# Kernel tuning notes

Measured on AMD Instinct MI355X. Metric: run time of the kernel, lower is better.

Reference implementation:

```python
import jax, jax.numpy as jnp
import numpy as np


def _ln(x, g, b, eps=1e-5):
    m = x.mean(-1, keepdims=True)
    v = x.var(-1, keepdims=True)
    return (x - m) / jnp.sqrt(v + eps) * g + b


def setup_inputs() -> dict:
    key = jax.random.key(0)
    ks = iter(jax.random.split(key, 48))
    B, N, H, Ld, L, FF = 2048, 10, 256, 8, 4, 1024
    def w(shape, s=0.02):
        return jax.random.normal(next(ks), shape, jnp.float32) * s
    return dict(
        latent_code=jax.random.normal(next(ks), (B, Ld), jnp.float32),
        target_node_types=jax.random.randint(next(ks), (B, N), 0, 5),
        ce_w1=w((Ld, H)), ce_b1=jnp.zeros(H), ce_g1=jnp.ones(H), ce_be1=jnp.zeros(H),
        ce_w2=w((H, H)), ce_b2=jnp.zeros(H), ce_g2=jnp.ones(H), ce_be2=jnp.zeros(H),
        nc_w1=w((2, H // 4)), nc_b1=jnp.zeros(H // 4), nc_w2=w((H // 4, 3)), nc_b2=jnp.zeros(3),
        type_emb=w((5, H), 1.0), pos_emb=w((N, H), 0.02),
        qkvo_w=w((L, 4, H, H)), qkvo_b=jnp.zeros((L, 4, H)),
        ln_g=jnp.ones((L, 2, H)), ln_b=jnp.zeros((L, 2, H)),
        ffn_w1=w((L, H, FF)), ffn_b1=jnp.zeros((L, FF)),
        ffn_w2=w((L, FF, H)), ffn_b2=jnp.zeros((L, H)),
        out_w=w((H, 5)), out_b=jnp.zeros(5),
        edge_w1=w((2 * H + Ld, H)), edge_b1=jnp.zeros(H),
        edge_w2=w((H, 8)), edge_b2=jnp.zeros(8),
    )


def reference(latent_code, target_node_types,
              ce_w1, ce_b1, ce_g1, ce_be1, ce_w2, ce_b2, ce_g2, ce_be2,
              nc_w1, nc_b1, nc_w2, nc_b2,
              type_emb, pos_emb, qkvo_w, qkvo_b, ln_g, ln_b,
              ffn_w1, ffn_b1, ffn_w2, ffn_b2, out_w, out_b,
              edge_w1, edge_b1, edge_w2, edge_b2):
    B, Ld = latent_code.shape
    N = target_node_types.shape[1]
    H = ce_w1.shape[1]
    L = qkvo_w.shape[0]
    nh = 8
    hd = H // nh

    # context encoder: Linear -> LN -> ReLU -> Linear -> LN
    h0 = jax.nn.relu(_ln(latent_code @ ce_w1 + ce_b1, ce_g1, ce_be1))
    context = _ln(h0 @ ce_w2 + ce_b2, ce_g2, ce_be2)  # [B,H]

    # node count head on latent_code[:, :2]
    node_count_logits = jax.nn.relu(latent_code[:, :2] @ nc_w1 + nc_b1) @ nc_w2 + nc_b2  # [B,3]

    # teacher-forced node embeddings (independent of predictions -> vectorizable)
    ne = type_emb[target_node_types] + pos_emb[:N]          # [B,N,H]
    h = context[:, None, :] + pos_emb[:N]                   # queries [B,N,H]
    mem = jnp.concatenate([context[:, None, :], ne], axis=1)  # keys [B,N+1,H]
    # position i attends to context (k=0) and nodes j<i (k=j+1), i.e. k <= i
    kmask = (jnp.arange(N + 1)[None, :] <= jnp.arange(N)[:, None])  # [N,N+1]
    scale = 1.0 / np.sqrt(hd).astype(np.float32)

    for l in range(L):
        Q = (h @ qkvo_w[l, 0] + qkvo_b[l, 0]).reshape(B, N, nh, hd)
        K = (mem @ qkvo_w[l, 1] + qkvo_b[l, 1]).reshape(B, N + 1, nh, hd)
        V = (mem @ qkvo_w[l, 2] + qkvo_b[l, 2]).reshape(B, N + 1, nh, hd)
        s = jnp.einsum('bnhd,bmhd->bhnm', Q, K) * scale
        s = jnp.where(kmask[None, None], s, jnp.float32(-1e9))
        a = jax.nn.softmax(s, axis=-1)
        o = jnp.einsum('bhnm,bmhd->bnhd', a, V).reshape(B, N, H)
        h = _ln(h + o @ qkvo_w[l, 3] + qkvo_b[l, 3], ln_g[l, 0], ln_b[l, 0])
        f = jax.nn.relu(h @ ffn_w1[l] + ffn_b1[l]) @ ffn_w2[l] + ffn_b2[l]
        h = _ln(h + f, ln_g[l, 1], ln_b[l, 1])

    node_logits = h @ out_w + out_b  # [B,N,5]

    # pairwise edge decoder on (emb_i, emb_j, latent) for i>j, symmetrized
    ei = jnp.broadcast_to(ne[:, :, None, :], (B, N, N, H))
    ej = jnp.broadcast_to(ne[:, None, :, :], (B, N, N, H))
    lat = jnp.broadcast_to(latent_code[:, None, None, :], (B, N, N, Ld))
    feat = jnp.concatenate([ei, ej, lat], axis=-1)  # [B,N,N,2H+Ld]
    elog = jax.nn.relu(feat @ edge_w1 + edge_b1) @ edge_w2 + edge_b2  # [B,N,N,8]
    tril = (jnp.arange(N)[:, None] > jnp.arange(N)[None, :])[None, :, :, None]
    lower = jnp.where(tril, elog, jnp.float32(0.0))
    edge_component_logits = lower + jnp.swapaxes(lower, 1, 2)  # diag stays zero

    return node_logits, node_count_logits, edge_component_logits
```

## Files before the change

kernel.cpp:

```cpp
#include <hip/hip_runtime.h>
#include <hip/hip_bf16.h>

#define BATCH 2048
#define NNODE 10
#define NLAYER 4
#define ROWS_H (BATCH*NNODE)
#define ROWS_M (BATCH*(NNODE+1))
#define KVSTR 2048

typedef __hip_bfloat16 bf16;
typedef unsigned short u16;
typedef unsigned int u32;
typedef __attribute__((ext_vector_type(8))) short bf16x8;
typedef __attribute__((ext_vector_type(4))) float f32x4;

__device__ __forceinline__ float bfb(u16 u) {
    union { u32 i; float f; } c; c.i = (u32)u << 16; return c.f;
}
__device__ __forceinline__ float bf2f(bf16 x) { return __bfloat162float(x); }
__device__ __forceinline__ bf16 f2bf(float x) { return __float2bfloat16(x); }
__device__ __forceinline__ u16 f2u(float v) {
    bf16 t = f2bf(v); u16 u; __builtin_memcpy(&u, &t, 2); return u;
}
__device__ __forceinline__ void store_out(void* out, int f32o, size_t idx, float v) {
    if (f32o) ((float*)out)[idx] = v; else ((bf16*)out)[idx] = f2bf(v);
}
__device__ __forceinline__ int dflag(const u32* g) { return g[0] == 0x3F800000u; }

#define GLL(src, dst) __builtin_amdgcn_global_load_lds( \
    (const __attribute__((address_space(1))) void*)(src), \
    (__attribute__((address_space(3))) void*)(dst), 16, 0, 0)

#define NT 26
struct CvtArgs { const void* src[NT]; int n[NT]; int off[NT]; };

__global__ __launch_bounds__(256) void cvt_kernel(CvtArgs a, bf16* __restrict__ dst,
                                                  const u32* __restrict__ gptr) {
    int f = dflag(gptr);
    int gid = blockIdx.x * 256 + threadIdx.x;
    int stride = gridDim.x * 256;
    for (int tn = 0; tn < NT; tn++) {
        const void* s = a.src[tn];
        bf16* d = dst + a.off[tn];
        int n = a.n[tn];
        if (f) {
            const float* sf = (const float*)s;
            for (int i = gid; i < n; i += stride) d[i] = f2bf(sf[i]);
        } else {
            const bf16* sb = (const bf16*)s;
            for (int i = gid; i < n; i += stride) d[i] = sb[i];
        }
    }
}

#define NTT 26
struct TTArgs {
    const void* src[NTT];
    int soff[NTT]; int doff[NTT]; int R[NTT]; int C[NTT];
    int tileStart[NTT];
    int nTiles;
};

__global__ __launch_bounds__(256) void tt_kernel(TTArgs a, u16* __restrict__ dst,
                                                 const u32* __restrict__ gptr) {
    int f = dflag(gptr);
    int bid = blockIdx.x;
    if (bid >= a.nTiles) return;
    int tn = 0;
    while (tn + 1 < NTT && a.tileStart[tn + 1] <= bid) tn++;
    int lt = bid - a.tileStart[tn];
    int R = a.R[tn], C = a.C[tn];
    int tilesC = C >> 6;
    int tr = lt / tilesC, tc = lt - tr * tilesC;

    __shared__ u16 Ts[64 * 66];
    int t = threadIdx.x;

    if (f) {
        const float* s = (const float*)a.src[tn] + a.soff[tn];
        #pragma unroll
        for (int it = 0; it < 16; it++) {
            int flat = it * 256 + t;
            int lr = flat >> 6, lc = flat & 63;
            Ts[lr * 66 + lc] = f2u(s[(size_t)(tr * 64 + lr) * C + tc * 64 + lc]);
        }
    } else {
        const u16* s = (const u16*)a.src[tn] + a.soff[tn];
        #pragma unroll
        for (int it = 0; it < 16; it++) {
            int flat = it * 256 + t;
            int lr = flat >> 6, lc = flat & 63;
            Ts[lr * 66 + lc] = s[(size_t)(tr * 64 + lr) * C + tc * 64 + lc];
        }
    }
    __syncthreads();

    u16* d = dst + a.doff[tn];
    #pragma unroll
    for (int it = 0; it < 16; it++) {
        int flat = it * 256 + t;
        int orow = flat >> 6, ocol = flat & 63;
        d[(size_t)(tc * 64 + orow) * R + tr * 64 + ocol] = Ts[ocol * 66 + orow];
    }
}

__global__ __launch_bounds__(256) void kvbias_kernel(const bf16* __restrict__ qb,
                                                     bf16* __restrict__ dst) {
    int t = blockIdx.x * 256 + threadIdx.x;
    if (t < 2048) {
        int l = t >> 9, c = t & 511;
        dst[t] = qb[(l * 4 + 1) * 256 + c];
    }
}

__device__ __forceinline__ void ln_stats256(float x, float* s_red, float& m, float& var) {
    float v1 = x, v2 = x * x;
    #pragma unroll
    for (int off = 32; off; off >>= 1) {
        v1 += __shfl_down(v1, off, 64);
        v2 += __shfl_down(v2, off, 64);
    }
    int wave = threadIdx.x >> 6, lane = threadIdx.x & 63;
    if (!lane) { s_red[wave] = v1; s_red[4 + wave] = v2; }
    __syncthreads();
    m   = (s_red[0] + s_red[1] + s_red[2] + s_red[3]) * (1.f / 256.f);
    var = (s_red[4] + s_red[5] + s_red[6] + s_red[7]) * (1.f / 256.f) - m * m;
    __syncthreads();
}

__global__ __launch_bounds__(256) void ctx_kernel(
    const bf16* __restrict__ lat_bf, const int* __restrict__ types,
    const bf16* __restrict__ ce_w1, const bf16* __restrict__ ce_b1,
    const bf16* __restrict__ ce_g1, const bf16* __restrict__ ce_be1,
    const bf16* __restrict__ ce_w2, const bf16* __restrict__ ce_b2,
    const bf16* __restrict__ ce_g2, const bf16* __restrict__ ce_be2,
    const bf16* __restrict__ nc_w1, const bf16* __restrict__ nc_b1,
    const bf16* __restrict__ nc_w2, const bf16* __restrict__ nc_b2,
    const bf16* __restrict__ type_emb, const bf16* __restrict__ pos_emb,
    const bf16* __restrict__ edge_w1, const bf16* __restrict__ edge_b1,
    bf16* __restrict__ h, bf16* __restrict__ mem, bf16* __restrict__ ne,
    bf16* __restrict__ rvec, void* __restrict__ out, const u32* __restrict__ gptr)
{
    int b = blockIdx.x;
    int t = threadIdx.x;
    int f32o = dflag(gptr);
    __shared__ float lat[8];
    __shared__ float s_h0[256];
    __shared__ float s_red[8];
    __shared__ float s_nc[64];

    if (t < 8) lat[t] = bf2f(lat_bf[b * 8 + t]);
    __syncthreads();

    float x = bf2f(ce_b1[t]);
    #pragma unroll
    for (int k = 0; k < 8; k++) x += lat[k] * bf2f(ce_w1[k * 256 + t]);
    float m, var;
    ln_stats256(x, s_red, m, var);
    float r = rsqrtf(var + 1e-5f);
    float h0 = fmaxf((x - m) * r * bf2f(ce_g1[t]) + bf2f(ce_be1[t]), 0.f);
    s_h0[t] = h0;
    __syncthreads();

    float x2 = bf2f(ce_b2[t]);
    for (int k = 0; k < 256; k++) x2 += s_h0[k] * bf2f(ce_w2[k * 256 + t]);
    ln_stats256(x2, s_red, m, var);
    r = rsqrtf(var + 1e-5f);
    float ctx = (x2 - m) * r * bf2f(ce_g2[t]) + bf2f(ce_be2[t]);

    mem[(size_t)(b * 11) * 256 + t] = f2bf(ctx);
    for (int n = 0; n < NNODE; n++) {
        float pe = bf2f(pos_emb[n * 256 + t]);
        h[(size_t)(b * NNODE + n) * 256 + t] = f2bf(ctx + pe);
        int ty = types[b * NNODE + n];
        float nv = bf2f(type_emb[ty * 256 + t]) + pe;
        ne[(size_t)(b * NNODE + n) * 256 + t] = f2bf(nv);
        mem[(size_t)(b * 11 + 1 + n) * 256 + t] = f2bf(nv);
    }

    float rv = bf2f(edge_b1[t]);
    #pragma unroll
    for (int k = 0; k < 8; k++) rv += lat[k] * bf2f(edge_w1[(512 + k) * 256 + t]);
    rvec[(size_t)b * 256 + t] = f2bf(rv);

    if (t < 64) {
        float hn = lat[0] * bf2f(nc_w1[t]) + lat[1] * bf2f(nc_w1[64 + t]) + bf2f(nc_b1[t]);
        s_nc[t] = fmaxf(hn, 0.f);
    }
    __syncthreads();
    if (t < 3) {
        float o = bf2f(nc_b2[t]);
        for (int k = 0; k < 64; k++) o += s_nc[k] * bf2f(nc_w2[k * 3 + t]);
        store_out(out, f32o, (size_t)102400 + b * 3 + t, o);
    }
}

__global__ __launch_bounds__(256) void gemm_mfma(
    const u16* __restrict__ A, const u16* __restrict__ Bt,
    const bf16* __restrict__ bias, bf16* __restrict__ C,
    int M, int K, int N, int act)
{
    __shared__ u16 Als[2][128 * 32];
    __shared__ u16 Bls[2][128 * 32];
    int t = threadIdx.x;
    int w = t >> 6, l = t & 63;
    int m0 = blockIdx.y * 128, n0 = blockIdx.x * 128;
    int wr = (w >> 1) * 64, wc = (w & 1) * 64;

    int srow = w * 32 + (l >> 2);
    int selem = (l & 3) * 8;
    const u16* Ag = A + (size_t)(m0 + srow) * K + selem;
    const u16* Bg = Bt + (size_t)(n0 + srow) * K + selem;

    f32x4 acc[4][4];
    #pragma unroll
    for (int i = 0; i < 4; i++)
        #pragma unroll
        for (int j = 0; j < 4; j++)
            acc[i][j] = (f32x4){0.f, 0.f, 0.f, 0.f};

    int koff = (l >> 4) * 8;
    int mrow = wr + (l & 15);
    int ncol = wc + (l & 15);

    for (int kt = 0; kt < K; kt += 64) {
        #pragma unroll
        for (int hh = 0; hh < 2; hh++) {
            const u16* ag = Ag + kt + hh * 32;
            const u16* bg = Bg + kt + hh * 32;
            GLL(ag, &Als[hh][w * 1024]);
            GLL(ag + (size_t)16 * K, &Als[hh][w * 1024 + 512]);
            GLL(bg, &Bls[hh][w * 1024]);
            GLL(bg + (size_t)16 * K, &Bls[hh][w * 1024 + 512]);
        }
        __syncthreads();

        #pragma unroll
        for (int hh = 0; hh < 2; hh++) {
            bf16x8 af[4], bfr[4];
            #pragma unroll
            for (int i = 0; i < 4; i++) {
                af[i]  = *(const bf16x8*)&Als[hh][(mrow + i * 16) * 32 + koff];
                bfr[i] = *(const bf16x8*)&Bls[hh][(ncol + i * 16) * 32 + koff];
            }
            #pragma unroll
            for (int i = 0; i < 4; i++)
                #pragma unroll
                for (int j = 0; j < 4; j++)
                    acc[i][j] = __builtin_amdgcn_mfma_f32_16x16x32_bf16(af[i], bfr[j], acc[i][j], 0, 0, 0);
        }
        __syncthreads();
    }

    int rbase = (l >> 4) * 4;
    #pragma unroll
    for (int i = 0; i < 4; i++) {
        int m = m0 + wr + i * 16 + rbase;
        #pragma unroll
        for (int j = 0; j < 4; j++) {
            int n = n0 + wc + j * 16 + (l & 15);
            float bv = bias ? bf2f(bias[n]) : 0.f;
            #pragma unroll
            for (int r = 0; r < 4; r++) {
                float v = acc[i][j][r] + bv;
                if (act) v = fmaxf(v, 0.f);
                C[(size_t)(m + r) * N + n] = f2bf(v);
            }
        }
    }
}

template<int MODE>
__global__ __launch_bounds__(256) void gemm256(
    const u16* __restrict__ A, const u16* __restrict__ Bt,
    const bf16* __restrict__ bias, const bf16* __restrict__ g,
    const bf16* __restrict__ be, u16* __restrict__ hio,
    u16* __restrict__ C, int K)
{
    __shared__ u16 Asl[32 * 32];
    __shared__ u16 Bsl[256 * 32];
    __shared__ float lnp[2][4][32];
    int t = threadIdx.x, w = t >> 6, l = t & 63, q = l >> 4, l15 = l & 15;
    int m0 = blockIdx.x * 32;

    const u16* Ag = A + (size_t)(m0 + w * 16 + (l >> 2)) * K + (l & 3) * 8;
    const u16* Bg = Bt + (size_t)(w * 64 + (l >> 2)) * K + (l & 3) * 8;

    f32x4 acc[2][4];
    #pragma unroll
    for (int i = 0; i < 2; i++)
        #pragma unroll
        for (int j = 0; j < 4; j++)
            acc[i][j] = (f32x4){0.f, 0.f, 0.f, 0.f};

    for (int kt = 0; kt < K; kt += 32) {
        if (w < 2) GLL(Ag + kt, &Asl[w * 512]);
        #pragma unroll
        for (int s = 0; s < 4; s++)
            GLL(Bg + kt + (size_t)(s * 16) * K, &Bsl[w * 2048 + s * 512]);
        __syncthreads();
        bf16x8 af[2], bfr[4];
        #pragma unroll
        for (int i = 0; i < 2; i++)
            af[i] = *(const bf16x8*)&Asl[(i * 16 + l15) * 32 + q * 8];
        #pragma unroll
        for (int j = 0; j < 4; j++)
            bfr[j] = *(const bf16x8*)&Bsl[(w * 64 + j * 16 + l15) * 32 + q * 8];
        #pragma unroll
        for (int i = 0; i < 2; i++)
            #pragma unroll
            for (int j = 0; j < 4; j++)
                acc[i][j] = __builtin_amdgcn_mfma_f32_16x16x32_bf16(af[i], bfr[j], acc[i][j], 0, 0, 0);
        __syncthreads();
    }

    float bv[4];
    #pragma unroll
    for (int j = 0; j < 4; j++) bv[j] = bf2f(bias[w * 64 + j * 16 + l15]);

    if (MODE == 0) {
        #pragma unroll
        for (int i = 0; i < 2; i++)
            #pragma unroll
            for (int r = 0; r < 4; r++) {
                int row = m0 + i * 16 + q * 4 + r;
                #pragma unroll
                for (int j = 0; j < 4; j++)
                    C[(size_t)row * 256 + w * 64 + j * 16 + l15] = f2u(acc[i][j][r] + bv[j]);
            }
    } else {
        float gv[4], bev[4];
        #pragma unroll
        for (int j = 0; j < 4; j++) {
            gv[j] = bf2f(g[w * 64 + j * 16 + l15]);
            bev[j] = bf2f(be[w * 64 + j * 16 + l15]);
        }
        #pragma unroll
        for (int i = 0; i < 2; i++)
            #pragma unroll
            for (int r = 0; r < 4; r++) {
                int row = m0 + i * 16 + q * 4 + r;
                float s = 0.f, s2 = 0.f;
                #pragma unroll
                for (int j = 0; j < 4; j++) {
                    float xv = acc[i][j][r] + bv[j] + bfb(hio[(size_t)row * 256 + w * 64 + j * 16 + l15]);
                    acc[i][j][r] = xv; s += xv; s2 += xv * xv;
                }
                #pragma unroll
                for (int d = 1; d < 16; d <<= 1) {
                    s  += __shfl_xor(s, d, 64);
                    s2 += __shfl_xor(s2, d, 64);
                }
                if (l15 == 0) {
                    lnp[0][w][i * 16 + q * 4 + r] = s;
                    lnp[1][w][i * 16 + q * 4 + r] = s2;
                }
            }
        __syncthreads();
        #pragma unroll
        for (int i = 0; i < 2; i++)
            #pragma unroll
            for (int r = 0; r < 4; r++) {
                int lr = i * 16 + q * 4 + r;
                float S  = lnp[0][0][lr] + lnp[0][1][lr] + lnp[0][2][lr] + lnp[0][3][lr];
                float S2 = lnp[1][0][lr] + lnp[1][1][lr] + lnp[1][2][lr] + lnp[1][3][lr];
                float mean = S * (1.f / 256.f);
                float var = S2 * (1.f / 256.f) - mean * mean;
                float rstd = rsqrtf(var + 1e-5f);
                #pragma unroll
                for (int j = 0; j < 4; j++)
                    hio[(size_t)(m0 + lr) * 256 + w * 64 + j * 16 + l15] =
                        f2u((acc[i][j][r] - mean) * rstd * gv[j] + bev[j]);
            }
    }
}

__global__ __launch_bounds__(512) void ffn_kernel(
    u16* __restrict__ h, const u16* __restrict__ W1T, const u16* __restrict__ W2T,
    const bf16* __restrict__ b1, const bf16* __restrict__ b2,
    const bf16* __restrict__ g, const bf16* __restrict__ be)
{
    __shared__ u16 Asl[32 * 268];
    __shared__ u16 W1s[128 * 32];
    __shared__ u16 mids[32 * 140];
    __shared__ u16 W2s[256 * 32];
    __shared__ float lnp[2][8][32];

    int t = threadIdx.x, w = t >> 6, l = t & 63, q = l >> 4, l15 = l & 15;
    int m0 = blockIdx.x * 32;

    {
        int row = t >> 4, seg = (t & 15) * 16;
        const u16* src = h + (size_t)(m0 + row) * 256 + seg;
        u16* dst = &Asl[row * 268 + seg];
        *(uint4*)(dst) = *(const uint4*)(src);
        *(uint4*)(dst + 8) = *(const uint4*)(src + 8);
    }

    f32x4 accO[2][2];
    #pragma unroll
    for (int i = 0; i < 2; i++)
        #pragma unroll
        for (int j = 0; j < 2; j++)
            accO[i][j] = (f32x4){0.f, 0.f, 0.f, 0.f};
    __syncthreads();

    for (int c = 0; c < 8; c++) {
        f32x4 accM[2];
        accM[0] = (f32x4){0.f, 0.f, 0.f, 0.f};
        accM[1] = (f32x4){0.f, 0.f, 0.f, 0.f};

        for (int kt = 0; kt < 256; kt += 32) {
            const u16* src = W1T + (size_t)(c * 128 + w * 16 + (l >> 2)) * 256 + kt + (l & 3) * 8;
            GLL(src, &W1s[w * 512]);
            __syncthreads();
            bf16x8 af[2], bfm;
            #pragma unroll
            for (int i = 0; i < 2; i++)
                af[i] = *(const bf16x8*)&Asl[(i * 16 + l15) * 268 + kt + q * 8];
            bfm = *(const bf16x8*)&W1s[(w * 16 + l15) * 32 + q * 8];
            #pragma unroll
            for (int i = 0; i < 2; i++)
                accM[i] = __builtin_amdgcn_mfma_f32_16x16x32_bf16(af[i], bfm, accM[i], 0, 0, 0);
            __syncthreads();
        }
        float b1v = bf2f(b1[c * 128 + w * 16 + l15]);
        #pragma unroll
        for (int i = 0; i < 2; i++)
            #pragma unroll
            for (int r = 0; r < 4; r++) {
                int row = i * 16 + q * 4 + r, col = w * 16 + l15;
                mids[row * 140 + col] = f2u(fmaxf(accM[i][r] + b1v, 0.f));
            }

        for (int kt2 = 0; kt2 < 4; kt2++) {
            const u16* src = W2T + (size_t)(w * 32 + (l >> 2)) * 1024 + c * 128 + kt2 * 32 + (l & 3) * 8;
            GLL(src, &W2s[w * 1024]);
            GLL(src + (size_t)16 * 1024, &W2s[w * 1024 + 512]);
            __syncthreads();
            bf16x8 am[2], bo[2];
            #pragma unroll
            for (int i = 0; i < 2; i++)
                am[i] = *(const bf16x8*)&mids[(i * 16 + l15) * 140 + kt2 * 32 + q * 8];
            #pragma unroll
            for (int j = 0; j < 2; j++)
                bo[j] = *(const bf16x8*)&W2s[(w * 32 + j * 16 + l15) * 32 + q * 8];
            #pragma unroll
            for (int i = 0; i < 2; i++)
                #pragma unroll
                for (int j = 0; j < 2; j++)
                    accO[i][j] = __builtin_amdgcn_mfma_f32_16x16x32_bf16(am[i], bo[j], accO[i][j], 0, 0, 0);
            __syncthreads();
        }
    }

    float b2v[2], gv[2], bev[2];
    #pragma unroll
    for (int j = 0; j < 2; j++) {
        int col = w * 32 + j * 16 + l15;
        b2v[j] = bf2f(b2[col]); gv[j] = bf2f(g[col]); bev[j] = bf2f(be[col]);
    }
    #pragma unroll
    for (int i = 0; i < 2; i++)
        #pragma unroll
        for (int r = 0; r < 4; r++) {
            int row = i * 16 + q * 4 + r;
            float s = 0.f, s2 = 0.f;
            #pragma unroll
            for (int j = 0; j < 2; j++) {
                float xv = accO[i][j][r] + b2v[j] + bfb(Asl[row * 268 + w * 32 + j * 16 + l15]);
                accO[i][j][r] = xv; s += xv; s2 += xv * xv;
            }
            #pragma unroll
            for (int d = 1; d < 16; d <<= 1) {
                s  += __shfl_xor(s, d, 64);
                s2 += __shfl_xor(s2, d, 64);
            }
            if (l15 == 0) { lnp[0][w][row] = s; lnp[1][w][row] = s2; }
        }
    __syncthreads();
    #pragma unroll
    for (int i = 0; i < 2; i++)
        #pragma unroll
        for (int r = 0; r < 4; r++) {
            int lr = i * 16 + q * 4 + r;
            float S = 0.f, S2 = 0.f;
            #pragma unroll
            for (int ww = 0; ww < 8; ww++) { S += lnp[0][ww][lr]; S2 += lnp[1][ww][lr]; }
            float mean = S * (1.f / 256.f);
            float var = S2 * (1.f / 256.f) - mean * mean;
            float rstd = rsqrtf(var + 1e-5f);
            #pragma unroll
            for (int j = 0; j < 2; j++)
                h[(size_t)(m0 + lr) * 256 + w * 32 + j * 16 + l15] =
                    f2u((accO[i][j][r] - mean) * rstd * gv[j] + bev[j]);
        }
}

__global__ __launch_bounds__(256) void attn_kernel(
    const bf16* __restrict__ Qb, const bf16* __restrict__ KVb,
    bf16* __restrict__ Ob)
{
    int b = blockIdx.x;
    int t = threadIdx.x;
    __shared__ float Qs[10 * 256];
    __shared__ float Ks[11 * 256];
    __shared__ float S[880];

    const u16* Qu = (const u16*)Qb + (size_t)b * 2560;
    for (int e = t; e < 640; e += 256) {
        ushort4 v = *(const ushort4*)(Qu + e * 4);
        int base = e * 4;
        Qs[base] = bfb(v.x); Qs[base + 1] = bfb(v.y);
        Qs[base + 2] = bfb(v.z); Qs[base + 3] = bfb(v.w);
    }
    const u16* KVu = (const u16*)KVb + (size_t)b * 11 * KVSTR;
    for (int e = t; e < 704; e += 256) {
        int k = e >> 6, off = (e & 63) * 4;
        ushort4 v = *(const ushort4*)(KVu + (size_t)k * KVSTR + off);
        float* dst = &Ks[k * 256 + off];
        dst[0] = bfb(v.x); dst[1] = bfb(v.y); dst[2] = bfb(v.z); dst[3] = bfb(v.w);
    }
    __syncthreads();

    const float scale = 0.17677669529663687f;
    for (int e = t; e < 880; e += 256) {
        int head = e / 110, rem = e % 110, i = rem / 11, k = rem % 11;
        if (k <= i) {
            const float* qp = &Qs[i * 256 + head * 32];
            const float* kp = &Ks[k * 256 + head * 32];
            float s = 0.f;
            #pragma unroll
            for (int d = 0; d < 32; d++) s += qp[d] * kp[d];
            S[e] = s * scale;
        }
    }
    __syncthreads();
    if (t < 80) {
        int head = t / 10, i = t % 10;
        float* row = &S[head * 110 + i * 11];
        float mx = -1e30f;
        for (int k = 0; k <= i; k++) mx = fmaxf(mx, row[k]);
        float sum = 0.f;
        for (int k = 0; k <= i; k++) { float e = __expf(row[k] - mx); row[k] = e; sum += e; }
        float inv = 1.f / sum;
        for (int k = 0; k <= i; k++) row[k] *= inv;
    }
    __syncthreads();

    int head = t >> 5;
    float o[10] = {0.f, 0.f, 0.f, 0.f, 0.f, 0.f, 0.f, 0.f, 0.f, 0.f};
    for (int k = 0; k < 11; k++) {
        float v = bf2f(((const bf16*)KVb)[(size_t)(b * 11 + k) * KVSTR + 256 + t]);
        for (int i = k; i < 10; i++) o[i] += S[head * 110 + i * 11 + k] * v;
    }
    for (int i = 0; i < 10; i++) Ob[(size_t)(b * 10 + i) * 256 + t] = f2bf(o[i]);
}

__global__ __launch_bounds__(256) void outhead_kernel(
    const bf16* __restrict__ h, const bf16* __restrict__ w,
    const bf16* __restrict__ b, void* __restrict__ out, const u32* __restrict__ gptr)
{
    int f32o = dflag(gptr);
    int wv = threadIdx.x >> 6, l = threadIdx.x & 63;
    size_t row = (size_t)blockIdx.x * 4 + wv;
    ushort4 hv = *(const ushort4*)((const u16*)h + row * 256 + l * 4);
    float x[4] = {bfb(hv.x), bfb(hv.y), bfb(hv.z), bfb(hv.w)};
    float a[5] = {0.f, 0.f, 0.f, 0.f, 0.f};
    #pragma unroll
    for (int c = 0; c < 4; c++) {
        #pragma unroll
        for (int o = 0; o < 5; o++) a[o] += x[c] * bf2f(w[(l * 4 + c) * 5 + o]);
    }
    #pragma unroll
    for (int off = 32; off; off >>= 1)
        #pragma unroll
        for (int o = 0; o < 5; o++) a[o] += __shfl_xor(a[o], off, 64);
    if (!l)
        #pragma unroll
        for (int o = 0; o < 5; o++)
            store_out(out, f32o, row * 5 + o, a[o] + bf2f(b[o]));
}

__global__ __launch_bounds__(256) void edge_kernel(
    const bf16* __restrict__ PQ, const bf16* __restrict__ rvec,
    const bf16* __restrict__ w2, const bf16* __restrict__ b2,
    void* __restrict__ out, const u32* __restrict__ gptr)
{
    int f32o = dflag(gptr);
    int t = threadIdx.x, w = t >> 6, l = t & 63;
    int b = blockIdx.x * 4 + w;
    const size_t ebase = 108544;

    __shared__ u16 Pl[4][10 * 260];
    __shared__ u16 Ql[4][10 * 260];
    __shared__ u16 Rl[4][256];
    __shared__ float Wl[256 * 8];

    const u16* pq = (const u16*)PQ + (size_t)b * 10 * 512;
    #pragma unroll
    for (int i = 0; i < 10; i++) {
        ushort4 pv = *(const ushort4*)(pq + i * 512 + l * 4);
        ushort4 qv = *(const ushort4*)(pq + i * 512 + 256 + l * 4);
        *(ushort4*)&Pl[w][i * 260 + l * 4] = pv;
        *(ushort4*)&Ql[w][i * 260 + l * 4] = qv;
    }
    *(ushort4*)&Rl[w][l * 4] = *(const ushort4*)((const u16*)rvec + (size_t)b * 256 + l * 4);
    {
        const u16* wp = (const u16*)w2 + t * 8;
        #pragma unroll
        for (int o = 0; o < 8; o++) Wl[t * 8 + o] = bfb(wp[o]);
    }
    __syncthreads();

    if (l >= 45 && l < 55) {
        int i = l - 45;
        size_t o0 = ebase + ((size_t)(b * 10 + i) * 10 + i) * 8;
        if (f32o) {
            float4 z = {0.f, 0.f, 0.f, 0.f};
            *(float4*)((float*)out + o0) = z;
            *(float4*)((float*)out + o0 + 4) = z;
        } else {
            uint4 z = {0u, 0u, 0u, 0u};
            *(uint4*)((u16*)out + o0) = z;
        }
    }
    if (l < 45) {
        int i = 1;
        while (i * (i + 1) / 2 <= l) i++;
        int j = l - i * (i - 1) / 2;
        float acc[8] = {0.f, 0.f, 0.f, 0.f, 0.f, 0.f, 0.f, 0.f};
        const u16* Pp = &Pl[w][i * 260];
        const u16* Qp = &Ql[w][j * 260];
        const u16* Rp = &Rl[w][0];
        for (int c = 0; c < 256; c += 4) {
            ushort4 pv = *(const ushort4*)(Pp + c);
            ushort4 qv = *(const ushort4*)(Qp + c);
            ushort4 rv = *(const ushort4*)(Rp + c);
            float hc[4];
            hc[0] = fmaxf(bfb(pv.x) + bfb(qv.x) + bfb(rv.x), 0.f);
            hc[1] = fmaxf(bfb(pv.y) + bfb(qv.y) + bfb(rv.y), 0.f);
            hc[2] = fmaxf(bfb(pv.z) + bfb(qv.z) + bfb(rv.z), 0.f);
            hc[3] = fmaxf(bfb(pv.w) + bfb(qv.w) + bfb(rv.w), 0.f);
            #pragma unroll
            for (int cc = 0; cc < 4; cc++) {
                const float* wp = &Wl[(c + cc) * 8];
                #pragma unroll
                for (int o = 0; o < 8; o++) acc[o] += hc[cc] * wp[o];
            }
        }
        float r8[8];
        #pragma unroll
        for (int o = 0; o < 8; o++) r8[o] = acc[o] + bf2f(b2[o]);
        size_t o0 = ebase + ((size_t)(b * 10 + i) * 10 + j) * 8;
        size_t o1 = ebase + ((size_t)(b * 10 + j) * 10 + i) * 8;
        if (f32o) {
            float4 v0 = {r8[0], r8[1], r8[2], r8[3]};
            float4 v1 = {r8[4], r8[5], r8[6], r8[7]};
            *(float4*)((float*)out + o0) = v0; *(float4*)((float*)out + o0 + 4) = v1;
            *(float4*)((float*)out + o1) = v0; *(float4*)((float*)out + o1 + 4) = v1;
        } else {
            uint4 pk;
            pk.x = (u32)f2u(r8[0]) | ((u32)f2u(r8[1]) << 16);
            pk.y = (u32)f2u(r8[2]) | ((u32)f2u(r8[3]) << 16);
            pk.z = (u32)f2u(r8[4]) | ((u32)f2u(r8[5]) << 16);
            pk.w = (u32)f2u(r8[6]) | ((u32)f2u(r8[7]) << 16);
            *(uint4*)((u16*)out + o0) = pk;
            *(uint4*)((u16*)out + o1) = pk;
        }
    }
}

extern "C" void kernel_launch(void* const* d_in, const int* in_sizes, int n_in,
                              void* d_out, int out_size, void* d_ws, size_t ws_size,
                              hipStream_t stream) {
    const int* types = (const int*)d_in[1];
    const u32* gptr = (const u32*)d_in[18];

    static const int kIdx[NT] = {0,2,3,4,5,6,7,8,9,10,11,12,13,14,15,17,18,19,21,23,24,25,26,27,28,29};
    static const int kSz[NT]  = {16384,2048,256,256,256,65536,256,256,256,128,64,192,3,1280,2560,
                                 4096,2048,2048,4096,1024,1280,5,133120,256,2048,8};
    bf16* wbf = (bf16*)d_ws;

    CvtArgs ca;
    const bf16* cv[30];
    int off = 0;
    for (int i = 0; i < NT; i++) {
        ca.src[i] = d_in[kIdx[i]];
        ca.n[i] = kSz[i];
        ca.off[i] = off;
        cv[kIdx[i]] = wbf + off;
        off = (off + kSz[i] + 7) & ~7;
    }

    size_t wtbase_e = ((size_t)off + 127) & ~(size_t)127;
    u16* wt = (u16*)wbf + wtbase_e;
    const int PERL = 655360;
    const int KVBASE = 4 * PERL;
    const int PQBASE = KVBASE + 524288;
    TTArgs ta;
    int tn = 0, tiles = 0;
    auto addT = [&](const void* src, int soff, int doff, int R, int C) {
        ta.src[tn] = src; ta.soff[tn] = soff; ta.doff[tn] = doff;
        ta.R[tn] = R; ta.C[tn] = C; ta.tileStart[tn] = tiles;
        tiles += (R >> 6) * (C >> 6); tn++;
    };
    for (int l = 0; l < NLAYER; l++) {
        int base = l * PERL;
        addT(d_in[16], (l * 4 + 0) * 65536, base,           256, 256);
        addT(d_in[16], (l * 4 + 3) * 65536, base + 65536,   256, 256);
        addT(d_in[20], l * 262144,          base + 131072,  256, 1024);
        addT(d_in[22], l * 262144,          base + 393216,  1024, 256);
        addT(d_in[16], (l * 4 + 1) * 65536, KVBASE + l * 131072,         256, 256);
        addT(d_in[16], (l * 4 + 2) * 65536, KVBASE + l * 131072 + 65536, 256, 256);
    }
    addT(d_in[26], 0,     PQBASE,         256, 256);
    addT(d_in[26], 65536, PQBASE + 65536, 256, 256);
    ta.nTiles = tiles;

    size_t actbase_e = wtbase_e + 3801088 + 128;

    size_t EH = (size_t)ROWS_H * 256, EM = (size_t)ROWS_M * 256;
    bf16* p = (bf16*)wbf + actbase_e;
    bf16* h      = p; p += EH;
    bf16* mem    = p; p += EM;
    bf16* ne     = p; p += EH;
    bf16* rvec   = p; p += (size_t)BATCH * 256;
    bf16* kvbias = p; p += 2048;
    bf16* span   = p; p += (size_t)ROWS_H * 1024;
    bf16* kv_all = p;
    bf16* qbuf = span;
    bf16* obuf = span + EH;
    bf16* pqbuf = span;

    cvt_kernel<<<256, 256, 0, stream>>>(ca, wbf, gptr);
    tt_kernel<<<tiles, 256, 0, stream>>>(ta, wt, gptr);

    ctx_kernel<<<BATCH, 256, 0, stream>>>(
        cv[0], types, cv[2], cv[3], cv[4], cv[5], cv[6], cv[7], cv[8], cv[9],
        cv[10], cv[11], cv[12], cv[13], cv[14], cv[15], cv[26], cv[27],
        h, mem, ne, rvec, d_out, gptr);
    kvbias_kernel<<<8, 256, 0, stream>>>(cv[17], kvbias);

    gemm_mfma<<<dim3(16, ROWS_M / 128), 256, 0, stream>>>(
        (const u16*)mem, wt + KVBASE, kvbias, kv_all, ROWS_M, 256, 2048, 0);

    for (int l = 0; l < NLAYER; l++) {
        const u16* qT  = wt + (size_t)l * PERL;
        const u16* oT  = qT + 65536;
        const u16* f1T = qT + 131072;
        const u16* f2T = qT + 393216;
        const bf16* bq = cv[17] + (size_t)(l * 4 + 0) * 256;
        const bf16* bo = cv[17] + (size_t)(l * 4 + 3) * 256;
        const bf16* g1 = cv[18] + (size_t)(l * 2) * 256, *be1 = cv[19] + (size_t)(l * 2) * 256;
        const bf16* g2 = cv[18] + (size_t)(l * 2 + 1) * 256, *be2 = cv[19] + (size_t)(l * 2 + 1) * 256;

        gemm256<0><<<ROWS_H / 32, 256, 0, stream>>>((const u16*)h, qT, bq, nullptr, nullptr,
                                                    nullptr, (u16*)qbuf, 256);
        attn_kernel<<<BATCH, 256, 0, stream>>>(qbuf, kv_all + (size_t)l * 512, obuf);
        gemm256<1><<<ROWS_H / 32, 256, 0, stream>>>((const u16*)obuf, oT, bo, g1, be1,
                                                    (u16*)h, nullptr, 256);
        ffn_kernel<<<ROWS_H / 32, 512, 0, stream>>>((u16*)h, f1T, f2T,
                                                    cv[21] + (size_t)l * 1024, cv[23] + (size_t)l * 256,
                                                    g2, be2);
    }

    outhead_kernel<<<ROWS_H / 4, 256, 0, stream>>>(h, cv[24], cv[25], d_out, gptr);

    gemm_mfma<<<dim3(4, ROWS_H / 128), 256, 0, stream>>>((const u16*)ne, wt + PQBASE, nullptr, pqbuf, ROWS_H, 256, 512, 0);
    edge_kernel<<<BATCH / 4, 256, 0, stream>>>(pqbuf, rvec, cv[28], cv[29], d_out, gptr);
}
```

Baseline: 763.9 us.

## Restructure FFN kernel so each wave owns full rows with register-resident A

The fused FFN kernel now processes 64 rows per block with 4 waves, each wave owning 16 complete rows across all 256 output columns. The A operand is held in registers instead of staged through shared memory. Each staged weight tile is reused across more MFMAs, and the LayerNorm reduction becomes an intra-wave shuffle with no cross-wave shared-memory pass. The trade-off is much higher register pressure (16 output accumulators, 8 intermediate accumulators, 8 A fragments per lane), which may lower occupancy. There are also half as many blocks (320), so fewer CUs may be busy.

```diff
diff --git a/kernel.cpp b/kernel.cpp
--- a/kernel.cpp
+++ b/kernel.cpp
@@ -375,126 +375,107 @@
     }
 }
 
-__global__ __launch_bounds__(512) void ffn_kernel(
+__global__ __launch_bounds__(256) void ffn_kernel(
     u16* __restrict__ h, const u16* __restrict__ W1T, const u16* __restrict__ W2T,
     const bf16* __restrict__ b1, const bf16* __restrict__ b2,
     const bf16* __restrict__ g, const bf16* __restrict__ be)
 {
-    __shared__ u16 Asl[32 * 268];
-    __shared__ u16 W1s[128 * 32];
-    __shared__ u16 mids[32 * 140];
+    __shared__ u16 W1s[2][128 * 32];
+    __shared__ u16 mids[64 * 136];
     __shared__ u16 W2s[256 * 32];
-    __shared__ float lnp[2][8][32];
-
     int t = threadIdx.x, w = t >> 6, l = t & 63, q = l >> 4, l15 = l & 15;
-    int m0 = blockIdx.x * 32;
-
+    int m0 = blockIdx.x * 64;
+    int myrow = w * 16 + l15;
+
+    bf16x8 af[8];
     {
-        int row = t >> 4, seg = (t & 15) * 16;
-        const u16* src = h + (size_t)(m0 + row) * 256 + seg;
-        u16* dst = &Asl[row * 268 + seg];
-        *(uint4*)(dst) = *(const uint4*)(src);
-        *(uint4*)(dst + 8) = *(const uint4*)(src + 8);
-    }
-
-    f32x4 accO[2][2];
-    #pragma unroll
-    for (int i = 0; i < 2; i++)
-        #pragma unroll
-        for (int j = 0; j < 2; j++)
-            accO[i][j] = (f32x4){0.f, 0.f, 0.f, 0.f};
-    __syncthreads();
+        const u16* hp = h + (size_t)(m0 + myrow) * 256 + q * 8;
+        #pragma unroll
+        for (int kc = 0; kc < 8; kc++)
+            af[kc] = *(const bf16x8*)(hp + kc * 32);
+    }
+
+    f32x4 accO[16];
+    #pragma unroll
+    for (int j = 0; j < 16; j++) accO[j] = (f32x4){0.f, 0.f, 0.f, 0.f};
 
     for (int c = 0; c < 8; c++) {
-        f32x4 accM[2];
-        accM[0] = (f32x4){0.f, 0.f, 0.f, 0.f};
-        accM[1] = (f32x4){0.f, 0.f, 0.f, 0.f};
-
-        for (int kt = 0; kt < 256; kt += 32) {
-            const u16* src = W1T + (size_t)(c * 128 + w * 16 + (l >> 2)) * 256 + kt + (l & 3) * 8;
-            GLL(src, &W1s[w * 512]);
+        f32x4 accM[8];
+        #pragma unroll
+        for (int j = 0; j < 8; j++) accM[j] = (f32x4){0.f, 0.f, 0.f, 0.f};
+
+        for (int kp = 0; kp < 4; kp++) {
+            #pragma unroll
+            for (int hh = 0; hh < 2; hh++) {
+                int kt = kp * 64 + hh * 32;
+                const u16* src = W1T + (size_t)(c * 128 + w * 16 + (l >> 2)) * 256 + kt + (l & 3) * 8;
+                GLL(src, &W1s[hh][w * 512]);
+                GLL(src + (size_t)64 * 256, &W1s[hh][2048 + w * 512]);
+            }
             __syncthreads();
-            bf16x8 af[2], bfm;
-            #pragma unroll
-            for (int i = 0; i < 2; i++)
-                af[i] = *(const bf16x8*)&Asl[(i * 16 + l15) * 268 + kt + q * 8];
-            bfm = *(const bf16x8*)&W1s[(w * 16 + l15) * 32 + q * 8];
-            #pragma unroll
-            for (int i = 0; i < 2; i++)
-                accM[i] = __builtin_amdgcn_mfma_f32_16x16x32_bf16(af[i], bfm, accM[i], 0, 0, 0);
+            #pragma unroll
+            for (int hh = 0; hh < 2; hh++) {
+                int kc = kp * 2 + hh;
+                #pragma unroll
+                for (int j = 0; j < 8; j++) {
+                    bf16x8 bfm = *(const bf16x8*)&W1s[hh][(j * 16 + l15) * 32 + q * 8];
+                    accM[j] = __builtin_amdgcn_mfma_f32_16x16x32_bf16(af[kc], bfm, accM[j], 0, 0, 0);
+                }
+            }
             __syncthreads();
         }
-        float b1v = bf2f(b1[c * 128 + w * 16 + l15]);
-        #pragma unroll
-        for (int i = 0; i < 2; i++)
-            #pragma unroll
-            for (int r = 0; r < 4; r++) {
-                int row = i * 16 + q * 4 + r, col = w * 16 + l15;
-                mids[row * 140 + col] = f2u(fmaxf(accM[i][r] + b1v, 0.f));
-            }
+        #pragma unroll
+        for (int j = 0; j < 8; j++) {
+            float b1v = bf2f(b1[c * 128 + j * 16 + l15]);
+            #pragma unroll
+            for (int r = 0; r < 4; r++)
+                mids[(w * 16 + q * 4 + r) * 136 + j * 16 + l15] =
+                    f2u(fmaxf(accM[j][r] + b1v, 0.f));
+        }
 
         for (int kt2 = 0; kt2 < 4; kt2++) {
-            const u16* src = W2T + (size_t)(w * 32 + (l >> 2)) * 1024 + c * 128 + kt2 * 32 + (l & 3) * 8;
-            GLL(src, &W2s[w * 1024]);
-            GLL(src + (size_t)16 * 1024, &W2s[w * 1024 + 512]);
+            const u16* src = W2T + (size_t)(w * 64 + (l >> 2)) * 1024 + c * 128 + kt2 * 32 + (l & 3) * 8;
+            #pragma unroll
+            for (int s = 0; s < 4; s++)
+                GLL(src + (size_t)(s * 16) * 1024, &W2s[w * 2048 + s * 512]);
             __syncthreads();
-            bf16x8 am[2], bo[2];
-            #pragma unroll
-            for (int i = 0; i < 2; i++)
-                am[i] = *(const bf16x8*)&mids[(i * 16 + l15) * 140 + kt2 * 32 + q * 8];
-            #pragma unroll
-            for (int j = 0; j < 2; j++)
-                bo[j] = *(const bf16x8*)&W2s[(w * 32 + j * 16 + l15) * 32 + q * 8];
-            #pragma unroll
-            for (int i = 0; i < 2; i++)
-                #pragma unroll
-                for (int j = 0; j < 2; j++)
-                    accO[i][j] = __builtin_amdgcn_mfma_f32_16x16x32_bf16(am[i], bo[j], accO[i][j], 0, 0, 0);
+            bf16x8 am = *(const bf16x8*)&mids[myrow * 136 + kt2 * 32 + q * 8];
+            #pragma unroll
+            for (int j = 0; j < 16; j++) {
+                bf16x8 bo = *(const bf16x8*)&W2s[(j * 16 + l15) * 32 + q * 8];
+                accO[j] = __builtin_amdgcn_mfma_f32_16x16x32_bf16(am, bo, accO[j], 0, 0, 0);
+            }
             __syncthreads();
         }
     }
 
-    float b2v[2], gv[2], bev[2];
-    #pragma unroll
-    for (int j = 0; j < 2; j++) {
-        int col = w * 32 + j * 16 + l15;
-        b2v[j] = bf2f(b2[col]); gv[j] = bf2f(g[col]); bev[j] = bf2f(be[col]);
-    }
-    #pragma unroll
-    for (int i = 0; i < 2; i++)
-        #pragma unroll
-        for (int r = 0; r < 4; r++) {
-            int row = i * 16 + q * 4 + r;
-            float s = 0.f, s2 = 0.f;
-            #pragma unroll
-            for (int j = 0; j < 2; j++) {
-                float xv = accO[i][j][r] + b2v[j] + bfb(Asl[row * 268 + w * 32 + j * 16 + l15]);
-                accO[i][j][r] = xv; s += xv; s2 += xv * xv;
-            }
-            #pragma unroll
-            for (int d = 1; d < 16; d <<= 1) {
-                s  += __shfl_xor(s, d, 64);
-                s2 += __shfl_xor(s2, d, 64);
-            }
-            if (l15 == 0) { lnp[0][w][row] = s; lnp[1][w][row] = s2; }
-        }
-    __syncthreads();
-    #pragma unroll
-    for (int i = 0; i < 2; i++)
-        #pragma unroll
-        for (int r = 0; r < 4; r++) {
-            int lr = i * 16 + q * 4 + r;
-            float S = 0.f, S2 = 0.f;
-            #pragma unroll
-            for (int ww = 0; ww < 8; ww++) { S += lnp[0][ww][lr]; S2 += lnp[1][ww][lr]; }
-            float mean = S * (1.f / 256.f);
-            float var = S2 * (1.f / 256.f) - mean * mean;
-            float rstd = rsqrtf(var + 1e-5f);
-            #pragma unroll
-            for (int j = 0; j < 2; j++)
-                h[(size_t)(m0 + lr) * 256 + w * 32 + j * 16 + l15] =
-                    f2u((accO[i][j][r] - mean) * rstd * gv[j] + bev[j]);
-        }
+    #pragma unroll
+    for (int r = 0; r < 4; r++) {
+        int row = m0 + w * 16 + q * 4 + r;
+        const u16* hr = h + (size_t)row * 256;
+        float xs[16];
+        float s = 0.f, s2 = 0.f;
+        #pragma unroll
+        for (int j = 0; j < 16; j++) {
+            int col = j * 16 + l15;
+            float xv = accO[j][r] + bf2f(b2[col]) + bfb(hr[col]);
+            xs[j] = xv; s += xv; s2 += xv * xv;
+        }
+        #pragma unroll
+        for (int d = 1; d < 16; d <<= 1) {
+            s  += __shfl_xor(s, d, 64);
+            s2 += __shfl_xor(s2, d, 64);
+        }
+        float mean = s * (1.f / 256.f);
+        float var = s2 * (1.f / 256.f) - mean * mean;
+        float rstd = rsqrtf(var + 1e-5f);
+        u16* hw = h + (size_t)row * 256;
+        #pragma unroll
+        for (int j = 0; j < 16; j++) {
+            int col = j * 16 + l15;
+            hw[col] = f2u((xs[j] - mean) * rstd * bf2f(g[col]) + bf2f(be[col]));
+        }
+    }
 }
 
 __global__ __launch_bounds__(256) void attn_kernel(
@@ -760,7 +741,7 @@
         attn_kernel<<<BATCH, 256, 0, stream>>>(qbuf, kv_all + (size_t)l * 512, obuf);
         gemm256<1><<<ROWS_H / 32, 256, 0, stream>>>((const u16*)obuf, oT, bo, g1, be1,
                                                     (u16*)h, nullptr, 256);
-        ffn_kernel<<<ROWS_H / 32, 512, 0, stream>>>((u16*)h, f1T, f2T,
+        ffn_kernel<<<ROWS_H / 64, 256, 0, stream>>>((u16*)h, f1T, f2T,
                                                     cv[21] + (size_t)l * 1024, cv[23] + (size_t)l * 256,
                                                     g2, be2);
     }
```

After: 943.4 us. 23.5% more time.
